# Kernel tuning notes

Hardware: AMD Instinct MI355X
Metric: run time of the kernel (lower is better)

The kernel has to match this reference:

```python
import jax, jax.numpy as jnp
import numpy as np

B, T, D = 2, 2048, 1024
H, DK, DV = 16, 64, 64
DFF = 4096
CONV = 4
EPS = 1e-6


def _layernorm(x):
    # elementwise_affine=False LayerNorm
    mu = jnp.mean(x, axis=-1, keepdims=True)
    xc = x - mu
    return xc * jax.lax.rsqrt(jnp.mean(xc * xc, axis=-1, keepdims=True) + EPS)


def _l2norm(x):
    return x * jax.lax.rsqrt(jnp.sum(x * x, axis=-1, keepdims=True) + EPS)


def _modulate(x, shift, scale):
    return x * (1.0 + scale[:, None, :]) + shift[:, None, :]


def _short_conv(x, w):
    # causal depthwise conv1d (kernel CONV) + SiLU; x: [B,T,Dc], w: [Dc,CONV]
    Tn = x.shape[1]
    xp = jnp.pad(x, ((0, 0), (CONV - 1, 0), (0, 0)))
    y = xp[:, 0:Tn, :] * w[:, 0]
    for i in range(1, CONV):
        y = y + xp[:, i:i + Tn, :] * w[:, i]
    return jax.nn.silu(y)


def _delta_rule(q, k, v, beta):
    # delta-rule linear-attention recurrence (fused_recurrent form)
    # q,k: [B,T,H,DK], v: [B,T,H,DV], beta: [B,T,H]
    scale = DK ** -0.5
    qs = jnp.moveaxis(q * scale, 1, 0)
    ks = jnp.moveaxis(k, 1, 0)
    vs = jnp.moveaxis(v, 1, 0)
    bs = jnp.moveaxis(beta, 1, 0)
    S0 = jnp.zeros((q.shape[0], H, DK, DV), q.dtype)

    def step(S, inp):
        qt, kt, vt, bt = inp
        pred = jnp.einsum('bhk,bhkv->bhv', kt, S)        # k_t^T S
        delta = bt[..., None] * (vt - pred)              # beta_t (v_t - k_t^T S)
        S = S + jnp.einsum('bhk,bhv->bhkv', kt, delta)   # rank-1 delta update
        o = jnp.einsum('bhk,bhkv->bhv', qt, S)
        return S, o

    _, o = jax.lax.scan(step, S0, (qs, ks, vs, bs))
    return jnp.moveaxis(o, 0, 1)  # [B,T,H,DV]


def _deltanet(xm, Wq, Wk, Wv, Wb, wcq, wck, wcv, w_onorm, Wo):
    Bb, Tn, Dd = xm.shape
    q = _short_conv(xm @ Wq, wcq)
    k = _short_conv(xm @ Wk, wck)
    v = _short_conv(xm @ Wv, wcv)
    beta = jax.nn.sigmoid(xm @ Wb)                        # [B,T,H]
    q = _l2norm(q.reshape(Bb, Tn, H, DK))
    k = _l2norm(k.reshape(Bb, Tn, H, DK))
    v = v.reshape(Bb, Tn, H, DV)
    o = _delta_rule(q, k, v, beta)
    # per-head RMSNorm output norm
    o = o * jax.lax.rsqrt(jnp.mean(o * o, axis=-1, keepdims=True) + EPS) * w_onorm
    return o.reshape(Bb, Tn, Dd) @ Wo


def setup_inputs():
    key = jax.random.key(0)
    ks = jax.random.split(key, 20)
    s = 0.02
    return {
        "x": jax.random.normal(ks[0], (B, T, D), jnp.float32),
        "c": jax.random.normal(ks[1], (B, D), jnp.float32),
        "W_ada": jax.random.normal(ks[2], (D, 6 * D), jnp.float32) * s,
        "b_ada": jnp.zeros((6 * D,), jnp.float32),
        "Wq": jax.random.normal(ks[3], (D, H * DK), jnp.float32) * s,
        "Wk": jax.random.normal(ks[4], (D, H * DK), jnp.float32) * s,
        "Wv": jax.random.normal(ks[5], (D, H * DV), jnp.float32) * s,
        "Wb": jax.random.normal(ks[6], (D, H), jnp.float32) * s,
        "wcq": jax.random.normal(ks[7], (H * DK, CONV), jnp.float32) * 0.5,
        "wck": jax.random.normal(ks[8], (H * DK, CONV), jnp.float32) * 0.5,
        "wcv": jax.random.normal(ks[9], (H * DV, CONV), jnp.float32) * 0.5,
        "w_onorm": jnp.ones((DV,), jnp.float32),
        "Wo": jax.random.normal(ks[10], (H * DV, D), jnp.float32) * s,
        "W1": jax.random.normal(ks[11], (D, DFF), jnp.float32) * s,
        "b1": jnp.zeros((DFF,), jnp.float32),
        "W2": jax.random.normal(ks[12], (DFF, D), jnp.float32) * s,
        "b2": jnp.zeros((D,), jnp.float32),
    }


def reference(x, c, W_ada, b_ada, Wq, Wk, Wv, Wb, wcq, wck, wcv, w_onorm, Wo, W1, b1, W2, b2):
    mods = jax.nn.silu(c) @ W_ada + b_ada
    sh_a, sc_a, g_a, sh_m, sc_m, g_m = jnp.split(mods, 6, axis=-1)
    attn_out = _deltanet(_modulate(_layernorm(x), sh_a, sc_a),
                         Wq, Wk, Wv, Wb, wcq, wck, wcv, w_onorm, Wo)
    x = x + g_a[:, None, :] * attn_out
    h = _modulate(_layernorm(x), sh_m, sc_m)
    mlp = jax.nn.gelu(h @ W1 + b1, approximate=True) @ W2 + b2
    return x + g_m[:, None, :] * mlp
```

## Files before the change

### kernel.cpp

```cpp
#include <hip/hip_runtime.h>
#include <math.h>

typedef __attribute__((ext_vector_type(4))) float f32x4;
typedef __attribute__((ext_vector_type(8))) short bf16x8;
typedef __attribute__((ext_vector_type(4))) short s16x4;

__device__ __forceinline__ short f2bf(float f) {
  union { float f; unsigned u; } c; c.f = f;
  unsigned r = c.u + 0x7FFFu + ((c.u >> 16) & 1u);
  return (short)(r >> 16);
}
__device__ __forceinline__ float bf2f(short b) {
  union { unsigned u; float f; } c;
  c.u = ((unsigned)(unsigned short)b) << 16;
  return c.f;
}
__device__ __forceinline__ f32x4 mfma16(bf16x8 a, bf16x8 b, f32x4 c) {
  return __builtin_amdgcn_mfma_f32_16x16x32_bf16(a, b, c, 0, 0, 0);
}
__device__ __forceinline__ void gload16(const short* g, short* l) {
  __builtin_amdgcn_global_load_lds(
      (const __attribute__((address_space(1))) unsigned int*)g,
      (__attribute__((address_space(3))) unsigned int*)l, 16, 0, 0);
}

__global__ void k_transpose_bf16(const float* __restrict__ in, short* __restrict__ out,
                                 int K, int N) {
  __shared__ float tile[32][33];
  int n0 = blockIdx.x * 32, k0 = blockIdx.y * 32;
  int tx = threadIdx.x & 31, ty = threadIdx.x >> 5;
  for (int i = ty; i < 32; i += 8) tile[i][tx] = in[(long)(k0 + i) * N + n0 + tx];
  __syncthreads();
  for (int i = ty; i < 32; i += 8) out[(long)(n0 + i) * K + k0 + tx] = f2bf(tile[tx][i]);
}

__global__ void k_transpose_wb(const float* __restrict__ Wb, short* __restrict__ WbT) {
  int idx = blockIdx.x * 256 + threadIdx.x;
  int n = idx >> 10, k = idx & 1023;
  WbT[n * 1024 + k] = f2bf(Wb[k * 16 + n]);
}

__global__ void k_mods_p1(const float* __restrict__ c, const float* __restrict__ W_ada,
                          float* __restrict__ part) {
  int cx = blockIdx.x, dc = blockIdx.y, tid = threadIdx.x;
  __shared__ float s0[128], s1[128];
  if (tid < 128) {
    float v = c[dc * 128 + tid];
    s0[tid] = v / (1.f + expf(-v));
  } else {
    int t = tid - 128;
    float v = c[1024 + dc * 128 + t];
    s1[t] = v / (1.f + expf(-v));
  }
  __syncthreads();
  int col = cx * 256 + tid;
  float a0 = 0.f, a1 = 0.f;
  const float* wp = W_ada + (long)(dc * 128) * 6144 + col;
  for (int d = 0; d < 128; d++) {
    float w = wp[(long)d * 6144];
    a0 += s0[d] * w;
    a1 += s1[d] * w;
  }
  part[((long)dc * 2) * 6144 + col] = a0;
  part[((long)dc * 2 + 1) * 6144 + col] = a1;
}
__global__ void k_mods_p2(const float* __restrict__ part, const float* __restrict__ b_ada,
                          float* __restrict__ mods) {
  int col = blockIdx.x * 256 + threadIdx.x;
  float a0 = 0.f, a1 = 0.f;
  for (int dc = 0; dc < 8; dc++) {
    a0 += part[((long)dc * 2) * 6144 + col];
    a1 += part[((long)dc * 2 + 1) * 6144 + col];
  }
  float b = b_ada[col];
  mods[col] = a0 + b;
  mods[6144 + col] = a1 + b;
}

__global__ void k_ln_mod(const float* __restrict__ x, const float* __restrict__ mods,
                         short* __restrict__ out, int sh_off, int sc_off) {
  int row = blockIdx.x, tid = threadIdx.x, b = row >> 11;
  float4 v = ((const float4*)(x + (long)row * 1024))[tid];
  float s = v.x + v.y + v.z + v.w;
  float ss = v.x * v.x + v.y * v.y + v.z * v.z + v.w * v.w;
  #pragma unroll
  for (int off = 1; off < 64; off <<= 1) { s += __shfl_xor(s, off); ss += __shfl_xor(ss, off); }
  __shared__ float rs[4], rq[4];
  if ((tid & 63) == 0) { rs[tid >> 6] = s; rq[tid >> 6] = ss; }
  __syncthreads();
  s = rs[0] + rs[1] + rs[2] + rs[3];
  ss = rq[0] + rq[1] + rq[2] + rq[3];
  float mu = s * (1.f / 1024.f);
  float rstd = rsqrtf(ss * (1.f / 1024.f) - mu * mu + 1e-6f);
  const float* shv = mods + b * 6144 + sh_off;
  const float* scv = mods + b * 6144 + sc_off;
  int c0 = tid * 4;
  float xs[4] = {v.x, v.y, v.z, v.w};
  s16x4 ov;
  #pragma unroll
  for (int j = 0; j < 4; j++)
    ov[j] = f2bf((xs[j] - mu) * rstd * (1.f + scv[c0 + j]) + shv[c0 + j]);
  ((s16x4*)(out + (long)row * 1024))[tid] = ov;
}

__global__ __launch_bounds__(256) void k_beta_mfma(
    const short* __restrict__ xm, const short* __restrict__ WbT,
    float* __restrict__ beta) {
  int tid = threadIdx.x, w = tid >> 6, l = tid & 63;
  int lr = l & 15, lg = l >> 4;
  int row0 = blockIdx.x * 64 + w * 16;
  const short* ap = xm + (long)(row0 + lr) * 1024 + lg * 8;
  const short* bp = WbT + lr * 1024 + lg * 8;
  f32x4 acc = (f32x4){0.f, 0.f, 0.f, 0.f};
  #pragma unroll 8
  for (int kk = 0; kk < 1024; kk += 32) {
    bf16x8 a = *(const bf16x8*)(ap + kk);
    bf16x8 b = *(const bf16x8*)(bp + kk);
    acc = mfma16(a, b, acc);
  }
  #pragma unroll
  for (int i = 0; i < 4; i++) {
    int row = row0 + lg * 4 + i;
    beta[row * 16 + lr] = 1.f / (1.f + expf(-acc[i]));
  }
}

__global__ __launch_bounds__(384) void k_conv3(
    const short* __restrict__ qkv, const float* __restrict__ wcq,
    const float* __restrict__ wck, const float* __restrict__ wcv,
    short* __restrict__ qbf, short* __restrict__ kb, short* __restrict__ vb) {
  int row = blockIdx.x, tid = threadIdx.x, t = row & 2047;
  int c0 = tid * 8;
  int seg = c0 >> 10;
  int lc = c0 & 1023;
  const float* wseg = (seg == 0) ? wcq : (seg == 1) ? wck : wcv;
  float xr[4][8];
  #pragma unroll
  for (int i = 0; i < 4; i++) {
    int tt = t - 3 + i;
    if (tt >= 0) {
      bf16x8 v = *(const bf16x8*)(qkv + (long)(row - 3 + i) * 3072 + c0);
      #pragma unroll
      for (int j = 0; j < 8; j++) xr[i][j] = bf2f(v[j]);
    } else {
      #pragma unroll
      for (int j = 0; j < 8; j++) xr[i][j] = 0.f;
    }
  }
  float y[8];
  #pragma unroll
  for (int j = 0; j < 8; j++) {
    float4 wv = *(const float4*)(wseg + (long)(lc + j) * 4);
    float a = xr[0][j] * wv.x + xr[1][j] * wv.y + xr[2][j] * wv.z + xr[3][j] * wv.w;
    y[j] = a / (1.f + __expf(-a));
  }
  if (seg < 2) {
    float ssq = 0.f;
    #pragma unroll
    for (int j = 0; j < 8; j++) ssq += y[j] * y[j];
    #pragma unroll
    for (int off = 1; off < 8; off <<= 1) ssq += __shfl_xor(ssq, off);
    float r = rsqrtf(ssq + 1e-6f) * ((seg == 0) ? 0.125f : 1.f);
    #pragma unroll
    for (int j = 0; j < 8; j++) y[j] *= r;
  }
  bf16x8 ov;
  #pragma unroll
  for (int j = 0; j < 8; j++) ov[j] = f2bf(y[j]);
  short* outp = (seg == 0) ? qbf : (seg == 1) ? kb : vb;
  *(bf16x8*)(outp + (long)row * 1024 + lc) = ov;
}

__global__ __launch_bounds__(256) void k_phaseA(
    const short* __restrict__ kb, const short* __restrict__ vb,
    const short* __restrict__ qbf, const float* __restrict__ beta,
    short* __restrict__ Wc, short* __restrict__ UTc,
    short* __restrict__ Lc, short* __restrict__ KTc) {
  int chunk = blockIdx.x, chain = blockIdx.y;
  int b = chain >> 4, h = chain & 15;
  long rowbase = (long)b * 2048 + chunk * 64;
  int col0 = h * 64;
  long cb = ((long)chain * 32 + chunk) * 4096;
  __shared__ short Kb[64][72], KTb[64][72], VTb[64][72], Mb[64][72];
  __shared__ float Sf[64][65], Mf[64][65];
  __shared__ float Tl[4][16][20];
  __shared__ float bl[64];
  int tid = threadIdx.x, w = tid >> 6, l = tid & 63;
  int lr = l & 15, lg = l >> 4;

  for (int i = tid; i < 64 * 65; i += 256) (&Mf[0][0])[i] = 0.f;
  {
    int t = tid & 63, g = tid >> 6;
    if (tid < 64) bl[tid] = beta[(rowbase + tid) * 16 + h];
    int dk0 = g * 16;
    bf16x8 kv0 = *(const bf16x8*)(kb + (rowbase + t) * 1024 + col0 + dk0);
    bf16x8 kv1 = *(const bf16x8*)(kb + (rowbase + t) * 1024 + col0 + dk0 + 8);
    bf16x8 vv0 = *(const bf16x8*)(vb + (rowbase + t) * 1024 + col0 + dk0);
    bf16x8 vv1 = *(const bf16x8*)(vb + (rowbase + t) * 1024 + col0 + dk0 + 8);
    *(bf16x8*)&Kb[t][dk0] = kv0;
    *(bf16x8*)&Kb[t][dk0 + 8] = kv1;
    #pragma unroll
    for (int j = 0; j < 8; j++) {
      KTb[dk0 + j][t] = kv0[j];
      KTb[dk0 + 8 + j][t] = kv1[j];
      VTb[dk0 + j][t] = vv0[j];
      VTb[dk0 + 8 + j][t] = vv1[j];
    }
  }
  __syncthreads();
  {
    bf16x8 af0 = *(const bf16x8*)&Kb[w * 16 + lr][lg * 8];
    bf16x8 af1 = *(const bf16x8*)&Kb[w * 16 + lr][32 + lg * 8];
    #pragma unroll
    for (int nt = 0; nt < 4; nt++) {
      f32x4 acc = (f32x4){0.f, 0.f, 0.f, 0.f};
      acc = mfma16(af0, *(const bf16x8*)&Kb[nt * 16 + lr][lg * 8], acc);
      acc = mfma16(af1, *(const bf16x8*)&Kb[nt * 16 + lr][32 + lg * 8], acc);
      #pragma unroll
      for (int i = 0; i < 4; i++) {
        int row = w * 16 + lg * 4 + i, col = nt * 16 + lr;
        Sf[row][col] = (col < row) ? bl[row] * acc[i] : 0.f;
      }
    }
  }
  __syncthreads();
  if (w == 0) {
    int blk = l >> 4, colc = l & 15, base = blk * 16;
    float mcol[16];
    #pragma unroll
    for (int r = 0; r < 16; r++) {
      float s = (r == colc) ? 1.f : 0.f;
      #pragma unroll
      for (int j = 0; j < 16; j++)
        if (j < r) s -= Sf[base + r][base + j] * mcol[j];
      mcol[r] = s;
    }
    #pragma unroll
    for (int r = 0; r < 16; r++) Mf[base + r][base + colc] = mcol[r];
  } else if (w <= 2) {
    int idx = (w - 1) * 64 + l;
    #pragma unroll
    for (int i = 0; i < 4; i++) {
      int v = idx * 4 + i, row = v >> 3, cg = (v & 7) * 8;
      *(bf16x8*)&KTc[cb + row * 64 + cg] = *(const bf16x8*)&KTb[row][cg];
    }
  }
  __syncthreads();
  if (w < 3) {
    int j = w;
    int r = l & 15, c4 = (l >> 4) * 4;
    for (int i = j + 1; i < 4; i++) {
      float t4[4] = {0.f, 0.f, 0.f, 0.f};
      for (int k = j; k < i; k++) {
        #pragma unroll
        for (int m = 0; m < 16; m++) {
          float a = Sf[i * 16 + r][k * 16 + m];
          #pragma unroll
          for (int ii = 0; ii < 4; ii++)
            t4[ii] += a * Mf[k * 16 + m][j * 16 + c4 + ii];
        }
      }
      #pragma unroll
      for (int ii = 0; ii < 4; ii++) Tl[w][r][c4 + ii] = t4[ii];
      float o4[4] = {0.f, 0.f, 0.f, 0.f};
      #pragma unroll
      for (int m = 0; m < 16; m++) {
        float d = Mf[i * 16 + r][i * 16 + m];
        #pragma unroll
        for (int ii = 0; ii < 4; ii++) o4[ii] += d * Tl[w][m][c4 + ii];
      }
      #pragma unroll
      for (int ii = 0; ii < 4; ii++) Mf[i * 16 + r][j * 16 + c4 + ii] = -o4[ii];
    }
  }
  __syncthreads();
  {
    int r = tid >> 2, c0 = (tid & 3) * 16;
    #pragma unroll
    for (int j2 = 0; j2 < 16; j2++)
      Mb[r][c0 + j2] = f2bf(Mf[r][c0 + j2] * bl[c0 + j2]);
  }
  __syncthreads();
  {
    bf16x8 am0 = *(const bf16x8*)&Mb[w * 16 + lr][lg * 8];
    bf16x8 am1 = *(const bf16x8*)&Mb[w * 16 + lr][32 + lg * 8];
    bf16x8 av0 = *(const bf16x8*)&VTb[w * 16 + lr][lg * 8];
    bf16x8 av1 = *(const bf16x8*)&VTb[w * 16 + lr][32 + lg * 8];
    long qoff = (rowbase + w * 16 + lr) * 1024 + col0 + lg * 8;
    bf16x8 aq0 = *(const bf16x8*)&qbf[qoff];
    bf16x8 aq1 = *(const bf16x8*)&qbf[qoff + 32];
    #pragma unroll
    for (int nt = 0; nt < 4; nt++) {
      f32x4 wa = (f32x4){0.f, 0.f, 0.f, 0.f};
      f32x4 ua = (f32x4){0.f, 0.f, 0.f, 0.f};
      f32x4 la = (f32x4){0.f, 0.f, 0.f, 0.f};
      wa = mfma16(am0, *(const bf16x8*)&KTb[nt * 16 + lr][lg * 8], wa);
      wa = mfma16(am1, *(const bf16x8*)&KTb[nt * 16 + lr][32 + lg * 8], wa);
      ua = mfma16(av0, *(const bf16x8*)&Mb[nt * 16 + lr][lg * 8], ua);
      ua = mfma16(av1, *(const bf16x8*)&Mb[nt * 16 + lr][32 + lg * 8], ua);
      la = mfma16(aq0, *(const bf16x8*)&Kb[nt * 16 + lr][lg * 8], la);
      la = mfma16(aq1, *(const bf16x8*)&Kb[nt * 16 + lr][32 + lg * 8], la);
      #pragma unroll
      for (int i = 0; i < 4; i++) {
        int row = w * 16 + lg * 4 + i, col = nt * 16 + lr;
        Wc[cb + row * 64 + col] = f2bf(wa[i]);
        UTc[cb + row * 64 + col] = f2bf(ua[i]);
        Lc[cb + row * 64 + col] = f2bf((col <= row) ? la[i] : 0.f);
      }
    }
  }
}

__global__ __launch_bounds__(256) void k_phaseB_seq(
    const short* __restrict__ Wc, const short* __restrict__ UTc,
    const short* __restrict__ KTc, short* __restrict__ STb, short* __restrict__ DTb) {
  int ds = blockIdx.x, chain = blockIdx.y;
  __shared__ short Wl[2][64][72];
  __shared__ short Kl[2][64][72];
  __shared__ short Ul[2][16][72];
  __shared__ float STf[16][68];
  __shared__ short Sb[16][72];
  __shared__ short DTl[16][72];
  int tid = threadIdx.x, w = tid >> 6, l = tid & 63;
  int lr = l & 15, lg = l >> 4;
  for (int i = tid; i < 16 * 68; i += 256) (&STf[0][0])[i] = 0.f;
  for (int i = tid; i < 16 * 72; i += 256) (&Sb[0][0])[i] = 0;
  int srow = tid >> 2, scol = (tid & 3) * 16;
  int ur = tid >> 4, uc = (tid & 15) * 4;
  bf16x8 wreg0, wreg1, kreg0, kreg1;
  s16x4 ureg;
  {
    long cb = (long)chain * 32 * 4096;
    wreg0 = *(const bf16x8*)&Wc[cb + srow * 64 + scol];
    wreg1 = *(const bf16x8*)&Wc[cb + srow * 64 + scol + 8];
    kreg0 = *(const bf16x8*)&KTc[cb + srow * 64 + scol];
    kreg1 = *(const bf16x8*)&KTc[cb + srow * 64 + scol + 8];
    ureg  = *(const s16x4*)&UTc[cb + (ds * 16 + ur) * 64 + uc];
  }
  *(bf16x8*)&Wl[0][srow][scol] = wreg0;
  *(bf16x8*)&Wl[0][srow][scol + 8] = wreg1;
  *(bf16x8*)&Kl[0][srow][scol] = kreg0;
  *(bf16x8*)&Kl[0][srow][scol + 8] = kreg1;
  *(s16x4*)&Ul[0][ur][uc] = ureg;
  __syncthreads();
  int cur = 0;
  for (int c = 0; c < 32; c++) {
    if (c + 1 < 32) {
      long cb = ((long)chain * 32 + c + 1) * 4096;
      wreg0 = *(const bf16x8*)&Wc[cb + srow * 64 + scol];
      wreg1 = *(const bf16x8*)&Wc[cb + srow * 64 + scol + 8];
      kreg0 = *(const bf16x8*)&KTc[cb + srow * 64 + scol];
      kreg1 = *(const bf16x8*)&KTc[cb + srow * 64 + scol + 8];
      ureg  = *(const s16x4*)&UTc[cb + (ds * 16 + ur) * 64 + uc];
    }
    {
      long so = (((long)chain * 32 + c) * 64 + ds * 16 + ur) * 64 + uc;
      *(s16x4*)&STb[so] = *(const s16x4*)&Sb[ur][uc];
    }
    bf16x8 afr0 = *(const bf16x8*)&Sb[lr][lg * 8];
    bf16x8 afr1 = *(const bf16x8*)&Sb[lr][32 + lg * 8];
    f32x4 dacc = (f32x4){0.f, 0.f, 0.f, 0.f};
    dacc = mfma16(afr0, *(const bf16x8*)&Wl[cur][w * 16 + lr][lg * 8], dacc);
    dacc = mfma16(afr1, *(const bf16x8*)&Wl[cur][w * 16 + lr][32 + lg * 8], dacc);
    #pragma unroll
    for (int i = 0; i < 4; i++) {
      int dv = lg * 4 + i, tt = w * 16 + lr;
      float u = bf2f(Ul[cur][dv][tt]);
      short d = f2bf(u - dacc[i]);
      DTl[dv][tt] = d;
      DTb[(((long)chain * 32 + c) * 64 + ds * 16 + dv) * 64 + tt] = d;
    }
    __syncthreads();
    bf16x8 ad0 = *(const bf16x8*)&DTl[lr][lg * 8];
    bf16x8 ad1 = *(const bf16x8*)&DTl[lr][32 + lg * 8];
    f32x4 sacc;
    #pragma unroll
    for (int i = 0; i < 4; i++) sacc[i] = STf[lg * 4 + i][w * 16 + lr];
    sacc = mfma16(ad0, *(const bf16x8*)&Kl[cur][w * 16 + lr][lg * 8], sacc);
    sacc = mfma16(ad1, *(const bf16x8*)&Kl[cur][w * 16 + lr][32 + lg * 8], sacc);
    #pragma unroll
    for (int i = 0; i < 4; i++) {
      STf[lg * 4 + i][w * 16 + lr] = sacc[i];
      Sb[lg * 4 + i][w * 16 + lr] = f2bf(sacc[i]);
    }
    __syncthreads();
    if (c + 1 < 32) {
      int nxt = cur ^ 1;
      *(bf16x8*)&Wl[nxt][srow][scol] = wreg0;
      *(bf16x8*)&Wl[nxt][srow][scol + 8] = wreg1;
      *(bf16x8*)&Kl[nxt][srow][scol] = kreg0;
      *(bf16x8*)&Kl[nxt][srow][scol + 8] = kreg1;
      *(s16x4*)&Ul[nxt][ur][uc] = ureg;
      cur = nxt;
      __syncthreads();
    }
  }
}

__global__ __launch_bounds__(256) void k_phaseBo(
    const short* __restrict__ STb, const short* __restrict__ DTb,
    const short* __restrict__ Lc, const short* __restrict__ qbf,
    const float* __restrict__ wn, short* __restrict__ on) {
  int chunk = blockIdx.x, chain = blockIdx.y;
  int b = chain >> 4, h = chain & 15;
  int tid = threadIdx.x, w = tid >> 6, l = tid & 63;
  int lr = l & 15, lg = l >> 4;
  long cb = ((long)chain * 32 + chunk) * 4096;
  long rowbase = (long)b * 2048 + chunk * 64;
  bf16x8 aq[2], alf[2];
  long qoff = (rowbase + w * 16 + lr) * 1024 + h * 64 + lg * 8;
  aq[0] = *(const bf16x8*)&qbf[qoff];
  aq[1] = *(const bf16x8*)&qbf[qoff + 32];
  alf[0] = *(const bf16x8*)&Lc[cb + (w * 16 + lr) * 64 + lg * 8];
  alf[1] = *(const bf16x8*)&Lc[cb + (w * 16 + lr) * 64 + 32 + lg * 8];
  f32x4 oacc[4];
  #pragma unroll
  for (int nt = 0; nt < 4; nt++) {
    oacc[nt] = (f32x4){0.f, 0.f, 0.f, 0.f};
    #pragma unroll
    for (int kk = 0; kk < 2; kk++) {
      bf16x8 bs = *(const bf16x8*)&STb[cb + (nt * 16 + lr) * 64 + kk * 32 + lg * 8];
      oacc[nt] = mfma16(aq[kk], bs, oacc[nt]);
      bf16x8 bd = *(const bf16x8*)&DTb[cb + (nt * 16 + lr) * 64 + kk * 32 + lg * 8];
      oacc[nt] = mfma16(alf[kk], bd, oacc[nt]);
    }
  }
  float ss[4];
  #pragma unroll
  for (int i = 0; i < 4; i++) {
    ss[i] = 0.f;
    #pragma unroll
    for (int nt = 0; nt < 4; nt++) ss[i] += oacc[nt][i] * oacc[nt][i];
  }
  #pragma unroll
  for (int off = 1; off < 16; off <<= 1) {
    #pragma unroll
    for (int i = 0; i < 4; i++) ss[i] += __shfl_xor(ss[i], off);
  }
  float rr[4];
  #pragma unroll
  for (int i = 0; i < 4; i++) rr[i] = rsqrtf(ss[i] * (1.f / 64.f) + 1e-6f);
  float wnv[4];
  #pragma unroll
  for (int nt = 0; nt < 4; nt++) wnv[nt] = wn[nt * 16 + lr];
  #pragma unroll
  for (int nt = 0; nt < 4; nt++) {
    #pragma unroll
    for (int i = 0; i < 4; i++) {
      long orow = rowbase + w * 16 + lg * 4 + i;
      on[orow * 1024 + h * 64 + nt * 16 + lr] = f2bf(oacc[nt][i] * rr[i] * wnv[nt]);
    }
  }
}

template <int EPI>
__device__ __forceinline__ void gemm_epi(float v, int row, int col, int N, void* C,
                                         const float* P1, const float* P2, const float* P3) {
  if (EPI == 0) {
    ((float*)C)[(long)row * N + col] = v;
  } else if (EPI == 1) {
    int bb = row >> 11;
    ((float*)C)[(long)row * N + col] = P1[(long)row * N + col] + P2[bb * 6144 + 2048 + col] * v;
  } else if (EPI == 2) {
    float t = v + P1[col];
    float y = 1.5957691216f * (t + 0.044715f * t * t * t);
    float g = t / (1.f + __expf(-y));
    ((short*)C)[(long)row * N + col] = f2bf(g);
  } else if (EPI == 3) {
    int bb = row >> 11;
    ((float*)C)[(long)row * N + col] =
        P1[(long)row * 1024 + col] + P2[bb * 6144 + 5120 + col] * (v + P3[col]);
  } else {
    ((short*)C)[(long)row * N + col] = f2bf(v);
  }
}

template <int EPI>
__global__ __launch_bounds__(512, 4) void k_gemm128(
    const short* __restrict__ A, const short* __restrict__ BT, void* __restrict__ C,
    int M, int N, int K,
    const float* __restrict__ P1, const float* __restrict__ P2, const float* __restrict__ P3) {
  __shared__ short As[2][128 * 64];
  __shared__ short Bs[2][128 * 64];
  int tid = threadIdx.x, w = tid >> 6, l = tid & 63;
  int lr = l & 15, lg = l >> 4;
  int wr = w >> 2, wc = w & 3;
  int nx = gridDim.x;
  int orig = blockIdx.y * nx + blockIdx.x;
  int cpx = (nx * gridDim.y) >> 3;
  int swz = (orig & 7) * cpx + (orig >> 3);
  int bx = swz % nx, by = swz / nx;
  int row0 = by * 128, col0 = bx * 128;
  int scol = ((l & 7) ^ (l >> 3)) * 8;
  const short* Ab = A + (long)(row0 + w * 8 + (l >> 3)) * K + scol;
  const short* Bb = BT + (long)(col0 + w * 8 + (l >> 3)) * K + scol;
  f32x4 acc[4][2];
  #pragma unroll
  for (int m = 0; m < 4; m++)
    #pragma unroll
    for (int n = 0; n < 2; n++) acc[m][n] = (f32x4){0.f, 0.f, 0.f, 0.f};
  int u0 = ((0 + lg) ^ (lr & 7)) * 8;
  int u1 = ((4 + lg) ^ (lr & 7)) * 8;

#define STAGE_G(buf, kt)                                                        \
  {                                                                             \
    _Pragma("unroll") for (int i = 0; i < 2; i++) {                             \
      gload16(Ab + (long)i * 64 * K + (kt), &As[buf][(i * 64 + w * 8) * 64]);   \
      gload16(Bb + (long)i * 64 * K + (kt), &Bs[buf][(i * 64 + w * 8) * 64]);   \
    }                                                                           \
  }
#define COMPUTE_G(buf)                                                          \
  {                                                                             \
    bf16x8 af[4], bv[2];                                                        \
    _Pragma("unroll") for (int m = 0; m < 4; m++)                               \
      af[m] = *(const bf16x8*)&As[buf][(wr * 64 + m * 16 + lr) * 64 + u0];      \
    _Pragma("unroll") for (int n = 0; n < 2; n++)                               \
      bv[n] = *(const bf16x8*)&Bs[buf][(wc * 32 + n * 16 + lr) * 64 + u0];      \
    _Pragma("unroll") for (int m = 0; m < 4; m++)                               \
      _Pragma("unroll") for (int n = 0; n < 2; n++)                             \
        acc[m][n] = mfma16(af[m], bv[n], acc[m][n]);                            \
    _Pragma("unroll") for (int m = 0; m < 4; m++)                               \
      af[m] = *(const bf16x8*)&As[buf][(wr * 64 + m * 16 + lr) * 64 + u1];      \
    _Pragma("unroll") for (int n = 0; n < 2; n++)                               \
      bv[n] = *(const bf16x8*)&Bs[buf][(wc * 32 + n * 16 + lr) * 64 + u1];      \
    _Pragma("unroll") for (int m = 0; m < 4; m++)                               \
      _Pragma("unroll") for (int n = 0; n < 2; n++)                             \
        acc[m][n] = mfma16(af[m], bv[n], acc[m][n]);                            \
  }

  STAGE_G(0, 0);
  __syncthreads();
  int cur = 0;
  int ktLast = K - 64;
  for (int kt = 0; kt < ktLast; kt += 64) {
    STAGE_G(cur ^ 1, kt + 64);
    COMPUTE_G(cur);
    __syncthreads();
    cur ^= 1;
  }
  COMPUTE_G(cur);
#undef STAGE_G
#undef COMPUTE_G

  #pragma unroll
  for (int m = 0; m < 4; m++)
    #pragma unroll
    for (int n = 0; n < 2; n++) {
      int col = col0 + wc * 32 + n * 16 + lr;
      #pragma unroll
      for (int i = 0; i < 4; i++)
        gemm_epi<EPI>(acc[m][n][i], row0 + wr * 64 + m * 16 + lg * 4 + i, col, N, C, P1, P2, P3);
    }
}

template <int EPI>
__global__ __launch_bounds__(512, 2) void k_gemm256(
    const short* __restrict__ A, const short* __restrict__ BT, void* __restrict__ C,
    int M, int N, int K,
    const float* __restrict__ P1, const float* __restrict__ P2, const float* __restrict__ P3) {
  __shared__ short As[2][256 * 64];
  __shared__ short Bs[2][256 * 64];
  int tid = threadIdx.x, w = tid >> 6, l = tid & 63;
  int lr = l & 15, lg = l >> 4;
  int wr = w >> 2, wc = w & 3;
  int nx = gridDim.x;
  int orig = blockIdx.y * nx + blockIdx.x;
  int cpx = (nx * gridDim.y) >> 3;
  int swz = (orig & 7) * cpx + (orig >> 3);
  int bx = swz % nx, by = swz / nx;
  int row0 = by * 256, col0 = bx * 256;
  int scol = ((l & 7) ^ (l >> 3)) * 8;
  const short* Ab = A + (long)(row0 + w * 8 + (l >> 3)) * K + scol;
  const short* Bb = BT + (long)(col0 + w * 8 + (l >> 3)) * K + scol;
  f32x4 acc[8][4];
  #pragma unroll
  for (int m = 0; m < 8; m++)
    #pragma unroll
    for (int n = 0; n < 4; n++) acc[m][n] = (f32x4){0.f, 0.f, 0.f, 0.f};
  int u0 = ((0 + lg) ^ (lr & 7)) * 8;
  int u1 = ((4 + lg) ^ (lr & 7)) * 8;

#define STAGE_G2(buf, kt)                                                       \
  {                                                                             \
    _Pragma("unroll") for (int i = 0; i < 4; i++) {                             \
      gload16(Ab + (long)i * 64 * K + (kt), &As[buf][(i * 64 + w * 8) * 64]);   \
      gload16(Bb + (long)i * 64 * K + (kt), &Bs[buf][(i * 64 + w * 8) * 64]);   \
    }                                                                           \
  }
#define COMPUTE_HALF2(buf, u)                                                   \
  {                                                                             \
    bf16x8 af[8], bv[4];                                                        \
    _Pragma("unroll") for (int m = 0; m < 8; m++)                               \
      af[m] = *(const bf16x8*)&As[buf][(wr * 128 + m * 16 + lr) * 64 + (u)];    \
    _Pragma("unroll") for (int n = 0; n < 4; n++)                               \
      bv[n] = *(const bf16x8*)&Bs[buf][(wc * 64 + n * 16 + lr) * 64 + (u)];     \
    _Pragma("unroll") for (int m = 0; m < 8; m++)                               \
      _Pragma("unroll") for (int n = 0; n < 4; n++)                             \
        acc[m][n] = mfma16(af[m], bv[n], acc[m][n]);                            \
  }

  STAGE_G2(0, 0);
  __syncthreads();
  int cur = 0;
  int ktLast = K - 64;
  for (int kt = 0; kt < ktLast; kt += 64) {
    STAGE_G2(cur ^ 1, kt + 64);
    COMPUTE_HALF2(cur, u0);
    COMPUTE_HALF2(cur, u1);
    __syncthreads();
    cur ^= 1;
  }
  COMPUTE_HALF2(cur, u0);
  COMPUTE_HALF2(cur, u1);
#undef STAGE_G2
#undef COMPUTE_HALF2

  #pragma unroll
  for (int m = 0; m < 8; m++)
    #pragma unroll
    for (int n = 0; n < 4; n++) {
      int col = col0 + wc * 64 + n * 16 + lr;
      #pragma unroll
      for (int i = 0; i < 4; i++)
        gemm_epi<EPI>(acc[m][n][i], row0 + wr * 128 + m * 16 + lg * 4 + i, col, N, C, P1, P2, P3);
    }
}

#define OFF_MODS  0L
#define OFF_MODSP 49152L
#define OFF_XM    442368L
#define OFF_QKV   8830976L
#define OFF_QBF   59162624L
#define OFF_KF    67551232L
#define OFF_VF    84328448L
#define OFF_BETA  101105664L
#define OFF_WC    101367808L
#define OFF_UT    109756416L
#define OFF_LC    118145024L
#define OFF_KT    126533632L
#define OFF_ON    134922240L
#define OFF_X2    143310848L
#define OFF_WQT   160088064L
#define OFF_WKT   162185216L
#define OFF_WVT   164282368L
#define OFF_WOT   166379520L
#define OFF_W1T   168476672L
#define OFF_W2T   176865280L
#define OFF_WBT   185253888L
#define OFF_STB   OFF_QKV
#define OFF_DTB   (OFF_QKV + 8388608L)
#define OFF_M1    (OFF_QKV + 16777216L)
#define OFF_H     OFF_XM

extern "C" void kernel_launch(void* const* d_in, const int* in_sizes, int n_in,
                              void* d_out, int out_size, void* d_ws, size_t ws_size,
                              hipStream_t stream) {
  const float* x     = (const float*)d_in[0];
  const float* c     = (const float*)d_in[1];
  const float* W_ada = (const float*)d_in[2];
  const float* b_ada = (const float*)d_in[3];
  const float* Wq    = (const float*)d_in[4];
  const float* Wk    = (const float*)d_in[5];
  const float* Wv    = (const float*)d_in[6];
  const float* Wb    = (const float*)d_in[7];
  const float* wcq   = (const float*)d_in[8];
  const float* wck   = (const float*)d_in[9];
  const float* wcv   = (const float*)d_in[10];
  const float* wn    = (const float*)d_in[11];
  const float* Wo    = (const float*)d_in[12];
  const float* W1    = (const float*)d_in[13];
  const float* b1    = (const float*)d_in[14];
  const float* W2    = (const float*)d_in[15];
  const float* b2    = (const float*)d_in[16];
  float* out = (float*)d_out;
  char* ws = (char*)d_ws;

  float* mods = (float*)(ws + OFF_MODS);
  float* modp = (float*)(ws + OFF_MODSP);
  short* xm   = (short*)(ws + OFF_XM);
  short* qkv  = (short*)(ws + OFF_QKV);
  short* qbf  = (short*)(ws + OFF_QBF);
  short* kb   = (short*)(ws + OFF_KF);
  short* vb   = (short*)(ws + OFF_VF);
  float* beta = (float*)(ws + OFF_BETA);
  short* Wc   = (short*)(ws + OFF_WC);
  short* UTc  = (short*)(ws + OFF_UT);
  short* Lc   = (short*)(ws + OFF_LC);
  short* KTc  = (short*)(ws + OFF_KT);
  short* STb  = (short*)(ws + OFF_STB);
  short* DTb  = (short*)(ws + OFF_DTB);
  short* on   = (short*)(ws + OFF_ON);
  float* x2   = (float*)(ws + OFF_X2);
  short* hbuf = (short*)(ws + OFF_H);
  short* m1   = (short*)(ws + OFF_M1);
  short* WqT  = (short*)(ws + OFF_WQT);
  short* WkT  = (short*)(ws + OFF_WKT);
  short* WvT  = (short*)(ws + OFF_WVT);
  short* WoT  = (short*)(ws + OFF_WOT);
  short* W1T  = (short*)(ws + OFF_W1T);
  short* W2T  = (short*)(ws + OFF_W2T);
  short* WbT  = (short*)(ws + OFF_WBT);

  k_transpose_bf16<<<dim3(32, 32), 256, 0, stream>>>(Wq, WqT, 1024, 1024);
  k_transpose_bf16<<<dim3(32, 32), 256, 0, stream>>>(Wk, WkT, 1024, 1024);
  k_transpose_bf16<<<dim3(32, 32), 256, 0, stream>>>(Wv, WvT, 1024, 1024);
  k_transpose_bf16<<<dim3(32, 32), 256, 0, stream>>>(Wo, WoT, 1024, 1024);
  k_transpose_bf16<<<dim3(128, 32), 256, 0, stream>>>(W1, W1T, 1024, 4096);
  k_transpose_bf16<<<dim3(32, 128), 256, 0, stream>>>(W2, W2T, 4096, 1024);
  k_transpose_wb<<<64, 256, 0, stream>>>(Wb, WbT);

  k_mods_p1<<<dim3(24, 8), 256, 0, stream>>>(c, W_ada, modp);
  k_mods_p2<<<24, 256, 0, stream>>>(modp, b_ada, mods);
  k_ln_mod<<<4096, 256, 0, stream>>>(x, mods, xm, 0, 1024);

  k_gemm128<4><<<dim3(24, 32), 512, 0, stream>>>(xm, WqT, qkv, 4096, 3072, 1024,
                                                 nullptr, nullptr, nullptr);
  k_beta_mfma<<<64, 256, 0, stream>>>(xm, WbT, beta);

  k_conv3<<<4096, 384, 0, stream>>>(qkv, wcq, wck, wcv, qbf, kb, vb);

  k_phaseA<<<dim3(32, 32), 256, 0, stream>>>(kb, vb, qbf, beta, Wc, UTc, Lc, KTc);
  k_phaseB_seq<<<dim3(4, 32), 256, 0, stream>>>(Wc, UTc, KTc, STb, DTb);
  k_phaseBo<<<dim3(32, 32), 256, 0, stream>>>(STb, DTb, Lc, qbf, wn, on);

  k_gemm128<1><<<dim3(8, 32), 512, 0, stream>>>(on, WoT, x2, 4096, 1024, 1024,
                                                x, mods, nullptr);

  k_ln_mod<<<4096, 256, 0, stream>>>(x2, mods, hbuf, 3072, 4096);
  k_gemm256<2><<<dim3(16, 16), 512, 0, stream>>>(hbuf, W1T, m1, 4096, 4096, 1024,
                                                 b1, nullptr, nullptr);
  k_gemm128<3><<<dim3(8, 32), 512, 0, stream>>>(m1, W2T, out, 4096, 1024, 4096,
                                                x2, mods, b2);
}
```

Before: 327.6 us.

## Restructure 256x256 GEMM main loop into four-phase interleaved load/compute pipeline

The W1 GEMM kernel now splits each K-tile into four quadrant phases. Each phase reads its LDS fragments, issues part of the next tile's global-to-LDS loads, waits on a partial vmcnt, and runs its MFMAs at raised wave priority between barriers. The aim is to spread global loads across the compute instead of issuing them all at once, and to cut the stall at the single per-tile syncthreads. In exchange there are more barriers per tile and hand-tuned vmcnt counts that must match the load ordering exactly.

```diff
diff --git a/kernel.cpp b/kernel.cpp
--- a/kernel.cpp
+++ b/kernel.cpp
@@ -554,7 +554,7 @@
 }
 
 template <int EPI>
-__global__ __launch_bounds__(512, 2) void k_gemm256(
+__global__ __launch_bounds__(512, 2) void k_gemm256p(
     const short* __restrict__ A, const short* __restrict__ BT, void* __restrict__ C,
     int M, int N, int K,
     const float* __restrict__ P1, const float* __restrict__ P2, const float* __restrict__ P3) {
@@ -570,8 +570,6 @@
   int bx = swz % nx, by = swz / nx;
   int row0 = by * 256, col0 = bx * 256;
   int scol = ((l & 7) ^ (l >> 3)) * 8;
-  const short* Ab = A + (long)(row0 + w * 8 + (l >> 3)) * K + scol;
-  const short* Bb = BT + (long)(col0 + w * 8 + (l >> 3)) * K + scol;
   f32x4 acc[8][4];
   #pragma unroll
   for (int m = 0; m < 8; m++)
@@ -579,41 +577,72 @@
     for (int n = 0; n < 4; n++) acc[m][n] = (f32x4){0.f, 0.f, 0.f, 0.f};
   int u0 = ((0 + lg) ^ (lr & 7)) * 8;
   int u1 = ((4 + lg) ^ (lr & 7)) * 8;
-
-#define STAGE_G2(buf, kt)                                                       \
-  {                                                                             \
-    _Pragma("unroll") for (int i = 0; i < 4; i++) {                             \
-      gload16(Ab + (long)i * 64 * K + (kt), &As[buf][(i * 64 + w * 8) * 64]);   \
-      gload16(Bb + (long)i * 64 * K + (kt), &Bs[buf][(i * 64 + w * 8) * 64]);   \
-    }                                                                           \
-  }
-#define COMPUTE_HALF2(buf, u)                                                   \
-  {                                                                             \
-    bf16x8 af[8], bv[4];                                                        \
-    _Pragma("unroll") for (int m = 0; m < 8; m++)                               \
-      af[m] = *(const bf16x8*)&As[buf][(wr * 128 + m * 16 + lr) * 64 + (u)];    \
-    _Pragma("unroll") for (int n = 0; n < 4; n++)                               \
-      bv[n] = *(const bf16x8*)&Bs[buf][(wc * 64 + n * 16 + lr) * 64 + (u)];     \
-    _Pragma("unroll") for (int m = 0; m < 8; m++)                               \
-      _Pragma("unroll") for (int n = 0; n < 4; n++)                             \
-        acc[m][n] = mfma16(af[m], bv[n], acc[m][n]);                            \
-  }
-
-  STAGE_G2(0, 0);
-  __syncthreads();
-  int cur = 0;
-  int ktLast = K - 64;
-  for (int kt = 0; kt < ktLast; kt += 64) {
-    STAGE_G2(cur ^ 1, kt + 64);
-    COMPUTE_HALF2(cur, u0);
-    COMPUTE_HALF2(cur, u1);
-    __syncthreads();
-    cur ^= 1;
-  }
-  COMPUTE_HALF2(cur, u0);
-  COMPUTE_HALF2(cur, u1);
-#undef STAGE_G2
-#undef COMPUTE_HALF2
+  int wh = w & 3, ws = w >> 2;
+
+#define STAGE_A(buf, kt, mq)                                                         \
+  gload16(A + (long)(row0 + (mq) * 64 + w * 8 + (l >> 3)) * K + (kt) + scol,         \
+          &As[buf][((mq) * 64 + w * 8) * 64]);                                       \
+  gload16(A + (long)(row0 + 128 + (mq) * 64 + w * 8 + (l >> 3)) * K + (kt) + scol,   \
+          &As[buf][(128 + (mq) * 64 + w * 8) * 64]);
+#define STAGE_B(buf, kt, nq)                                                         \
+  gload16(BT + (long)(col0 + ws * 64 + (nq) * 32 + wh * 8 + (l >> 3)) * K + (kt) + scol, \
+          &Bs[buf][(ws * 64 + (nq) * 32 + wh * 8) * 64]);                            \
+  gload16(BT + (long)(col0 + 128 + ws * 64 + (nq) * 32 + wh * 8 + (l >> 3)) * K + (kt) + scol, \
+          &Bs[buf][(128 + ws * 64 + (nq) * 32 + wh * 8) * 64]);
+
+#define PHASE(buf, mq, nq, STAGE_STMT, DO_VM)                                        \
+  {                                                                                  \
+    bf16x8 af[4][2], bv[2][2];                                                       \
+    _Pragma("unroll") for (int m = 0; m < 4; m++) {                                  \
+      af[m][0] = *(const bf16x8*)&As[buf][(wr * 128 + (mq) * 64 + m * 16 + lr) * 64 + u0]; \
+      af[m][1] = *(const bf16x8*)&As[buf][(wr * 128 + (mq) * 64 + m * 16 + lr) * 64 + u1]; \
+    }                                                                                \
+    _Pragma("unroll") for (int n = 0; n < 2; n++) {                                  \
+      bv[n][0] = *(const bf16x8*)&Bs[buf][(wc * 64 + (nq) * 32 + n * 16 + lr) * 64 + u0]; \
+      bv[n][1] = *(const bf16x8*)&Bs[buf][(wc * 64 + (nq) * 32 + n * 16 + lr) * 64 + u1]; \
+    }                                                                                \
+    STAGE_STMT;                                                                      \
+    if (DO_VM) asm volatile("s_waitcnt vmcnt(4)" : : : "memory");                    \
+    __builtin_amdgcn_s_barrier();                                                    \
+    __builtin_amdgcn_s_setprio(1);                                                   \
+    _Pragma("unroll") for (int m = 0; m < 4; m++)                                    \
+      _Pragma("unroll") for (int n = 0; n < 2; n++) {                                \
+        acc[(mq) * 4 + m][(nq) * 2 + n] =                                            \
+            mfma16(af[m][0], bv[n][0], acc[(mq) * 4 + m][(nq) * 2 + n]);             \
+        acc[(mq) * 4 + m][(nq) * 2 + n] =                                            \
+            mfma16(af[m][1], bv[n][1], acc[(mq) * 4 + m][(nq) * 2 + n]);             \
+      }                                                                              \
+    __builtin_amdgcn_s_setprio(0);                                                   \
+    __builtin_amdgcn_s_barrier();                                                    \
+  }
+
+  STAGE_A(0, 0, 0);
+  STAGE_B(0, 0, 0);
+  STAGE_B(0, 0, 1);
+  STAGE_A(0, 0, 1);
+  asm volatile("s_waitcnt vmcnt(4)" : : : "memory");
+  __builtin_amdgcn_s_barrier();
+
+  int buf = 0;
+  int NT = K >> 6;
+  for (int t = 0; t < NT - 1; t++) {
+    int kn = (t + 1) * 64;
+    int bn = buf ^ 1;
+    PHASE(buf, 0, 0, STAGE_A(bn, kn, 0), 1);
+    PHASE(buf, 0, 1, STAGE_B(bn, kn, 0), 1);
+    PHASE(buf, 1, 0, STAGE_B(bn, kn, 1), 0);
+    PHASE(buf, 1, 1, STAGE_A(bn, kn, 1), 1);
+    buf = bn;
+  }
+  asm volatile("s_waitcnt vmcnt(0)" : : : "memory");
+  __builtin_amdgcn_s_barrier();
+  PHASE(buf, 0, 0, (void)0, 0);
+  PHASE(buf, 0, 1, (void)0, 0);
+  PHASE(buf, 1, 0, (void)0, 0);
+  PHASE(buf, 1, 1, (void)0, 0);
+#undef PHASE
+#undef STAGE_A
+#undef STAGE_B
 
   #pragma unroll
   for (int m = 0; m < 8; m++)
@@ -727,8 +756,8 @@
                                                 x, mods, nullptr);
 
   k_ln_mod<<<4096, 256, 0, stream>>>(x2, mods, hbuf, 3072, 4096);
-  k_gemm256<2><<<dim3(16, 16), 512, 0, stream>>>(hbuf, W1T, m1, 4096, 4096, 1024,
-                                                 b1, nullptr, nullptr);
+  k_gemm256p<2><<<dim3(16, 16), 512, 0, stream>>>(hbuf, W1T, m1, 4096, 4096, 1024,
+                                                  b1, nullptr, nullptr);
   k_gemm128<3><<<dim3(8, 32), 512, 0, stream>>>(m1, W2T, out, 4096, 1024, 4096,
                                                 x2, mods, b2);
 }
```

After: 335.3 us. 2.3% more time.
